# Kernel optimization log

Measured on AMD Instinct MI355X. Metric: run time of the kernel, lower is better.

## Reference

```python
import jax, jax.numpy as jnp
import numpy as np

B, T, D = 4, 2048, 2048
NUM_EXPERTS = 64
TOP_K = 2


def setup_inputs() -> dict:
    key = jax.random.key(0)
    k_x, k_n, k_wg, k_wn = jax.random.split(key, 4)
    x = jax.random.normal(k_x, (B, T, D), dtype=jnp.float32)
    noise_eps = jax.random.normal(k_n, (B, T, NUM_EXPERTS), dtype=jnp.float32)
    # nn.Linear(D, E, bias=False): weight [E, D]; store transposed [D, E] for einsum
    scale = 1.0 / np.sqrt(D)
    w_gate = jax.random.uniform(k_wg, (D, NUM_EXPERTS), jnp.float32, -scale, scale)
    w_noise = jax.random.uniform(k_wn, (D, NUM_EXPERTS), jnp.float32, -scale, scale)
    return {"x": x, "noise_eps": noise_eps, "w_gate": w_gate, "w_noise": w_noise}


def reference(x, noise_eps, w_gate, w_noise):
    # gate + noisy logits: softplus(w_noise(x)) * randn_like (noise_eps passed in)
    logits = jnp.einsum("btd,de->bte", x, w_gate)
    noise = jax.nn.softplus(jnp.einsum("btd,de->bte", x, w_noise)) * noise_eps
    logits = logits + noise

    # top-k over experts
    top_k_logits, top_k_indices = jax.lax.top_k(logits, TOP_K)  # [B,T,K]

    # scatter(-inf fill) + softmax == softmax over top-k values scattered into E slots
    one_hot = jax.nn.one_hot(top_k_indices, NUM_EXPERTS, dtype=logits.dtype)  # [B,T,K,E]
    router_probs = jnp.einsum("btk,btke->bte", jax.nn.softmax(top_k_logits, axis=-1), one_hot)

    # per-expert mask: [num_tokens, K, E] -> permute(1,0,2) -> [K, num_tokens, E]
    exp_mask = one_hot.reshape(B * T, TOP_K, NUM_EXPERTS).transpose(1, 0, 2).astype(jnp.int32)
    return router_probs, top_k_indices, exp_mask
```

## Files before the change

kernel.cpp:

```cpp
#include <hip/hip_runtime.h>
#include <math.h>

#define DD     2048
#define EE     64
#define NTOK   8192
#define BM     32
#define KSPLIT 4
#define NKS    16

#define PROB_OFF 0
#define IDX_OFF  524288
#define MASK_OFF 540672
#define MASK_K_STRIDE (NTOK * EE)

typedef __bf16 bf16x8 __attribute__((ext_vector_type(8)));
typedef float  f32x16 __attribute__((ext_vector_type(16)));

__device__ __forceinline__ unsigned f2bf_rne(float f) {
  unsigned u = __float_as_uint(f);
  return (u + 0x7fffu + ((u >> 16) & 1u)) >> 16;
}
__device__ __forceinline__ float bf2f(unsigned h) {
  return __uint_as_float(h << 16);
}

__global__ __launch_bounds__(256) void prep_w(
    const float* __restrict__ wg, const float* __restrict__ wn,
    unsigned char* __restrict__ wsb)
{
  const int t  = blockIdx.x * 256 + threadIdx.x;
  const int l  = t & 63;
  const int nt = (t >> 6) & 3;
  const int g  = t >> 8;
  const int colg = nt * 32 + (l & 31);
  const int kb   = g * 16 + 8 * (l >> 5);
  const float* wsrc = (colg < EE) ? (wg + colg) : (wn + (colg - EE));

  unsigned hv[8], lv[8];
#pragma unroll
  for (int i = 0; i < 8; ++i) {
    const float v = wsrc[(size_t)(kb + i) * EE];
    const unsigned h = f2bf_rne(v);
    hv[i] = h;
    lv[i] = f2bf_rne(v - bf2f(h));
  }
  uint4 hq, lq;
  hq.x = hv[0] | (hv[1] << 16); hq.y = hv[2] | (hv[3] << 16);
  hq.z = hv[4] | (hv[5] << 16); hq.w = hv[6] | (hv[7] << 16);
  lq.x = lv[0] | (lv[1] << 16); lq.y = lv[2] | (lv[3] << 16);
  lq.z = lv[4] | (lv[5] << 16); lq.w = lv[6] | (lv[7] << 16);

  const size_t base = ((size_t)(g * 4 + nt) * 2) * 1024 + (size_t)l * 16;
  *reinterpret_cast<uint4*>(wsb + base)        = hq;
  *reinterpret_cast<uint4*>(wsb + base + 1024) = lq;
}

union BF8 { bf16x8 v; ushort u[8]; };

__device__ __forceinline__ void cvt_hilo(const float4& a, const float4& b,
                                         bf16x8& hi, bf16x8& lo) {
  const float f[8] = {a.x, a.y, a.z, a.w, b.x, b.y, b.z, b.w};
  BF8 H, L;
#pragma unroll
  for (int i = 0; i < 8; ++i) {
    const unsigned u = __float_as_uint(f[i]);
    H.u[i] = (ushort)(u >> 16);
    L.v[i] = (__bf16)(f[i] - __uint_as_float(u & 0xffff0000u));
  }
  hi = H.v; lo = L.v;
}

__device__ __forceinline__ bf16x8 bc(const uint4& q) {
  return __builtin_bit_cast(bf16x8, q);
}

__global__ __launch_bounds__(256, 4) void router_gemm(
    const float* __restrict__ x,
    const unsigned char* __restrict__ wsb,
    float* __restrict__ part)
{
  __shared__ float Lp[BM][128];

  const int tid  = threadIdx.x;
  const int w    = tid >> 6;
  const int lane = tid & 63;
  const int nt2  = w & 1;
  const int kq   = w >> 1;
  const int tok0 = blockIdx.x * BM;
  const int ks   = blockIdx.y;

  const int kbase = ks * 512 + kq * 256;
  const float* xp = x + (size_t)(tok0 + (lane & 31)) * DD
                      + kbase + 8 * (lane >> 5);
  const unsigned char* bp = wsb
      + ((size_t)((kbase >> 4) * 4 + 2 * nt2)) * 2048 + (size_t)lane * 16;

  f32x16 a0 = {0.f,0.f,0.f,0.f,0.f,0.f,0.f,0.f,0.f,0.f,0.f,0.f,0.f,0.f,0.f,0.f};
  f32x16 a1 = a0;

#pragma unroll
  for (int s = 0; s < NKS; ++s) {
    const float* p = xp + 16 * s;
    const float4 xa = *reinterpret_cast<const float4*>(p);
    const float4 xb = *reinterpret_cast<const float4*>(p + 4);
    const unsigned char* q = bp + (size_t)8192 * s;
    const uint4 bh0 = *reinterpret_cast<const uint4*>(q);
    const uint4 bl0 = *reinterpret_cast<const uint4*>(q + 1024);
    const uint4 bh1 = *reinterpret_cast<const uint4*>(q + 2048);
    const uint4 bl1 = *reinterpret_cast<const uint4*>(q + 3072);

    bf16x8 ahi, alo;
    cvt_hilo(xa, xb, ahi, alo);
    a0 = __builtin_amdgcn_mfma_f32_32x32x16_bf16(ahi, bc(bh0), a0, 0, 0, 0);
    a0 = __builtin_amdgcn_mfma_f32_32x32x16_bf16(ahi, bc(bl0), a0, 0, 0, 0);
    a0 = __builtin_amdgcn_mfma_f32_32x32x16_bf16(alo, bc(bh0), a0, 0, 0, 0);
    a1 = __builtin_amdgcn_mfma_f32_32x32x16_bf16(ahi, bc(bh1), a1, 0, 0, 0);
    a1 = __builtin_amdgcn_mfma_f32_32x32x16_bf16(ahi, bc(bl1), a1, 0, 0, 0);
    a1 = __builtin_amdgcn_mfma_f32_32x32x16_bf16(alo, bc(bh1), a1, 0, 0, 0);
  }

  const int ccol  = 64 * nt2 + (lane & 31);
  const int crow0 = 4 * (lane >> 5);
  if (kq == 0) {
#pragma unroll
    for (int q = 0; q < 16; ++q) {
      const int row = (q & 3) + 8 * (q >> 2) + crow0;
      Lp[row][ccol]      = a0[q];
      Lp[row][ccol + 32] = a1[q];
    }
  }
  __syncthreads();
  if (kq == 1) {
#pragma unroll
    for (int q = 0; q < 16; ++q) {
      const int row = (q & 3) + 8 * (q >> 2) + crow0;
      Lp[row][ccol]      += a0[q];
      Lp[row][ccol + 32] += a1[q];
    }
  }
  __syncthreads();

#pragma unroll
  for (int rr = 0; rr < 8; ++rr) {
    const int r = 8 * w + rr;
    const float2 v = *reinterpret_cast<const float2*>(&Lp[r][2 * lane]);
    *reinterpret_cast<float2*>(
        part + ((size_t)(tok0 + r) * KSPLIT + ks) * 128 + 2 * lane) = v;
  }
}

__global__ __launch_bounds__(256) void router_epilogue(
    const float* __restrict__ part,
    const float* __restrict__ noise_eps,
    float* __restrict__ out)
{
  const int t    = blockIdx.x * 4 + (threadIdx.x >> 6);
  const int lane = threadIdx.x & 63;

  const float* p = part + (size_t)t * KSPLIT * 128;
  float g = 0.0f, nraw = 0.0f;
#pragma unroll
  for (int s = 0; s < KSPLIT; ++s) {
    g    += p[s * 128 + lane];
    nraw += p[s * 128 + EE + lane];
  }
  const float ep = noise_eps[(size_t)t * EE + lane];

  const float sp = fmaxf(nraw, 0.0f) + log1pf(expf(-fabsf(nraw)));
  const float z  = fmaf(sp, ep, g);

  float v1 = z; int i1 = lane;
#pragma unroll
  for (int off = 32; off >= 1; off >>= 1) {
    const float ov = __shfl_xor(v1, off, 64);
    const int   oi = __shfl_xor(i1, off, 64);
    if (ov > v1 || (ov == v1 && oi < i1)) { v1 = ov; i1 = oi; }
  }
  float v2 = (lane == i1) ? -INFINITY : z; int i2 = lane;
#pragma unroll
  for (int off = 32; off >= 1; off >>= 1) {
    const float ov = __shfl_xor(v2, off, 64);
    const int   oi = __shfl_xor(i2, off, 64);
    if (ov > v2 || (ov == v2 && oi < i2)) { v2 = ov; i2 = oi; }
  }

  const float e2 = expf(v2 - v1);
  const float denom = 1.0f + e2;
  const float p1 = 1.0f / denom;
  const float p2 = e2 / denom;

  out[PROB_OFF + (size_t)t * EE + lane] =
      (lane == i1) ? p1 : ((lane == i2) ? p2 : 0.0f);

  if (lane == 0) {
    out[IDX_OFF + t * 2 + 0] = (float)i1;
    out[IDX_OFF + t * 2 + 1] = (float)i2;
  }

  out[MASK_OFF + 0 * MASK_K_STRIDE + (size_t)t * EE + lane] = (lane == i1) ? 1.0f : 0.0f;
  out[MASK_OFF + 1 * MASK_K_STRIDE + (size_t)t * EE + lane] = (lane == i2) ? 1.0f : 0.0f;
}

extern "C" void kernel_launch(void* const* d_in, const int* in_sizes, int n_in,
                              void* d_out, int out_size, void* d_ws, size_t ws_size,
                              hipStream_t stream) {
  const float* x   = (const float*)d_in[0];
  const float* eps = (const float*)d_in[1];
  const float* wg  = (const float*)d_in[2];
  const float* wn  = (const float*)d_in[3];

  unsigned char* wsb = (unsigned char*)d_ws;
  float* part = (float*)(wsb + (1 << 20));

  prep_w<<<dim3(128), dim3(256), 0, stream>>>(wg, wn, wsb);
  router_gemm<<<dim3(NTOK / BM, KSPLIT), dim3(256), 0, stream>>>(x, wsb, part);
  router_epilogue<<<dim3(NTOK / 4), dim3(256), 0, stream>>>(part, eps,
                                                            (float*)d_out);
}
```

Before: 137.1 us.

## Fuse router GEMM and top-k epilogue into one 1024-thread kernel

Merges the split-K GEMM and the top-k/softmax epilogue into a single kernel. Each 32-token block now uses 16 waves, each covering a 128-wide K slice and all 128 output columns. Partial sums are reduced through a 4-slab shared-memory buffer over four synchronised phases, after which each wave computes the epilogue for two tokens. This removes the global partial-sum buffer round trip and one kernel launch. In exchange it uses large 1024-thread blocks with more accumulator registers, which may lower occupancy, and adds four block barriers.

```diff
diff --git a/kernel.cpp b/kernel.cpp
--- a/kernel.cpp
+++ b/kernel.cpp
@@ -1,12 +1,12 @@
 #include <hip/hip_runtime.h>
 #include <math.h>
 
-#define DD     2048
-#define EE     64
-#define NTOK   8192
-#define BM     32
-#define KSPLIT 4
-#define NKS    16
+#define DD    2048
+#define EE    64
+#define NTOK  8192
+#define BM    32
+#define NKH   16
+#define NKS   8
 
 #define PROB_OFF 0
 #define IDX_OFF  524288
@@ -74,29 +74,26 @@
   return __builtin_bit_cast(bf16x8, q);
 }
 
-__global__ __launch_bounds__(256, 4) void router_gemm(
+__global__ __launch_bounds__(1024) void router_fused(
     const float* __restrict__ x,
+    const float* __restrict__ noise_eps,
     const unsigned char* __restrict__ wsb,
-    float* __restrict__ part)
+    float* __restrict__ out)
 {
-  __shared__ float Lp[BM][128];
+  __shared__ float Lp[4][BM][128];
 
   const int tid  = threadIdx.x;
-  const int w    = tid >> 6;
+  const int wid  = tid >> 6;
   const int lane = tid & 63;
-  const int nt2  = w & 1;
-  const int kq   = w >> 1;
+  const int kh   = wid;
   const int tok0 = blockIdx.x * BM;
-  const int ks   = blockIdx.y;
-
-  const int kbase = ks * 512 + kq * 256;
+
   const float* xp = x + (size_t)(tok0 + (lane & 31)) * DD
-                      + kbase + 8 * (lane >> 5);
-  const unsigned char* bp = wsb
-      + ((size_t)((kbase >> 4) * 4 + 2 * nt2)) * 2048 + (size_t)lane * 16;
+                      + kh * 128 + 8 * (lane >> 5);
+  const unsigned char* bp = wsb + (size_t)kh * 65536 + (size_t)lane * 16;
 
   f32x16 a0 = {0.f,0.f,0.f,0.f,0.f,0.f,0.f,0.f,0.f,0.f,0.f,0.f,0.f,0.f,0.f,0.f};
-  f32x16 a1 = a0;
+  f32x16 a1 = a0, a2 = a0, a3 = a0;
 
 #pragma unroll
   for (int s = 0; s < NKS; ++s) {
@@ -104,101 +101,111 @@
     const float4 xa = *reinterpret_cast<const float4*>(p);
     const float4 xb = *reinterpret_cast<const float4*>(p + 4);
     const unsigned char* q = bp + (size_t)8192 * s;
-    const uint4 bh0 = *reinterpret_cast<const uint4*>(q);
-    const uint4 bl0 = *reinterpret_cast<const uint4*>(q + 1024);
-    const uint4 bh1 = *reinterpret_cast<const uint4*>(q + 2048);
-    const uint4 bl1 = *reinterpret_cast<const uint4*>(q + 3072);
 
     bf16x8 ahi, alo;
     cvt_hilo(xa, xb, ahi, alo);
-    a0 = __builtin_amdgcn_mfma_f32_32x32x16_bf16(ahi, bc(bh0), a0, 0, 0, 0);
-    a0 = __builtin_amdgcn_mfma_f32_32x32x16_bf16(ahi, bc(bl0), a0, 0, 0, 0);
-    a0 = __builtin_amdgcn_mfma_f32_32x32x16_bf16(alo, bc(bh0), a0, 0, 0, 0);
-    a1 = __builtin_amdgcn_mfma_f32_32x32x16_bf16(ahi, bc(bh1), a1, 0, 0, 0);
-    a1 = __builtin_amdgcn_mfma_f32_32x32x16_bf16(ahi, bc(bl1), a1, 0, 0, 0);
-    a1 = __builtin_amdgcn_mfma_f32_32x32x16_bf16(alo, bc(bh1), a1, 0, 0, 0);
-  }
-
-  const int ccol  = 64 * nt2 + (lane & 31);
+
+    {
+      const uint4 bh0 = *reinterpret_cast<const uint4*>(q);
+      const uint4 bl0 = *reinterpret_cast<const uint4*>(q + 1024);
+      const uint4 bh1 = *reinterpret_cast<const uint4*>(q + 2048);
+      const uint4 bl1 = *reinterpret_cast<const uint4*>(q + 3072);
+      a0 = __builtin_amdgcn_mfma_f32_32x32x16_bf16(ahi, bc(bh0), a0, 0, 0, 0);
+      a0 = __builtin_amdgcn_mfma_f32_32x32x16_bf16(ahi, bc(bl0), a0, 0, 0, 0);
+      a0 = __builtin_amdgcn_mfma_f32_32x32x16_bf16(alo, bc(bh0), a0, 0, 0, 0);
+      a1 = __builtin_amdgcn_mfma_f32_32x32x16_bf16(ahi, bc(bh1), a1, 0, 0, 0);
+      a1 = __builtin_amdgcn_mfma_f32_32x32x16_bf16(ahi, bc(bl1), a1, 0, 0, 0);
+      a1 = __builtin_amdgcn_mfma_f32_32x32x16_bf16(alo, bc(bh1), a1, 0, 0, 0);
+    }
+    {
+      const uint4 bh2 = *reinterpret_cast<const uint4*>(q + 4096);
+      const uint4 bl2 = *reinterpret_cast<const uint4*>(q + 5120);
+      const uint4 bh3 = *reinterpret_cast<const uint4*>(q + 6144);
+      const uint4 bl3 = *reinterpret_cast<const uint4*>(q + 7168);
+      a2 = __builtin_amdgcn_mfma_f32_32x32x16_bf16(ahi, bc(bh2), a2, 0, 0, 0);
+      a2 = __builtin_amdgcn_mfma_f32_32x32x16_bf16(ahi, bc(bl2), a2, 0, 0, 0);
+      a2 = __builtin_amdgcn_mfma_f32_32x32x16_bf16(alo, bc(bh2), a2, 0, 0, 0);
+      a3 = __builtin_amdgcn_mfma_f32_32x32x16_bf16(ahi, bc(bh3), a3, 0, 0, 0);
+      a3 = __builtin_amdgcn_mfma_f32_32x32x16_bf16(ahi, bc(bl3), a3, 0, 0, 0);
+      a3 = __builtin_amdgcn_mfma_f32_32x32x16_bf16(alo, bc(bh3), a3, 0, 0, 0);
+    }
+  }
+
+  const int slab  = kh & 3;
+  const int phase = kh >> 2;
+  const int ccol  = lane & 31;
   const int crow0 = 4 * (lane >> 5);
-  if (kq == 0) {
-#pragma unroll
-    for (int q = 0; q < 16; ++q) {
-      const int row = (q & 3) + 8 * (q >> 2) + crow0;
-      Lp[row][ccol]      = a0[q];
-      Lp[row][ccol + 32] = a1[q];
-    }
-  }
-  __syncthreads();
-  if (kq == 1) {
-#pragma unroll
-    for (int q = 0; q < 16; ++q) {
-      const int row = (q & 3) + 8 * (q >> 2) + crow0;
-      Lp[row][ccol]      += a0[q];
-      Lp[row][ccol + 32] += a1[q];
-    }
-  }
-  __syncthreads();
-
-#pragma unroll
-  for (int rr = 0; rr < 8; ++rr) {
-    const int r = 8 * w + rr;
-    const float2 v = *reinterpret_cast<const float2*>(&Lp[r][2 * lane]);
-    *reinterpret_cast<float2*>(
-        part + ((size_t)(tok0 + r) * KSPLIT + ks) * 128 + 2 * lane) = v;
-  }
-}
-
-__global__ __launch_bounds__(256) void router_epilogue(
-    const float* __restrict__ part,
-    const float* __restrict__ noise_eps,
-    float* __restrict__ out)
-{
-  const int t    = blockIdx.x * 4 + (threadIdx.x >> 6);
-  const int lane = threadIdx.x & 63;
-
-  const float* p = part + (size_t)t * KSPLIT * 128;
-  float g = 0.0f, nraw = 0.0f;
-#pragma unroll
-  for (int s = 0; s < KSPLIT; ++s) {
-    g    += p[s * 128 + lane];
-    nraw += p[s * 128 + EE + lane];
-  }
-  const float ep = noise_eps[(size_t)t * EE + lane];
-
-  const float sp = fmaxf(nraw, 0.0f) + log1pf(expf(-fabsf(nraw)));
-  const float z  = fmaf(sp, ep, g);
-
-  float v1 = z; int i1 = lane;
-#pragma unroll
-  for (int off = 32; off >= 1; off >>= 1) {
-    const float ov = __shfl_xor(v1, off, 64);
-    const int   oi = __shfl_xor(i1, off, 64);
-    if (ov > v1 || (ov == v1 && oi < i1)) { v1 = ov; i1 = oi; }
-  }
-  float v2 = (lane == i1) ? -INFINITY : z; int i2 = lane;
-#pragma unroll
-  for (int off = 32; off >= 1; off >>= 1) {
-    const float ov = __shfl_xor(v2, off, 64);
-    const int   oi = __shfl_xor(i2, off, 64);
-    if (ov > v2 || (ov == v2 && oi < i2)) { v2 = ov; i2 = oi; }
-  }
-
-  const float e2 = expf(v2 - v1);
-  const float denom = 1.0f + e2;
-  const float p1 = 1.0f / denom;
-  const float p2 = e2 / denom;
-
-  out[PROB_OFF + (size_t)t * EE + lane] =
-      (lane == i1) ? p1 : ((lane == i2) ? p2 : 0.0f);
-
-  if (lane == 0) {
-    out[IDX_OFF + t * 2 + 0] = (float)i1;
-    out[IDX_OFF + t * 2 + 1] = (float)i2;
-  }
-
-  out[MASK_OFF + 0 * MASK_K_STRIDE + (size_t)t * EE + lane] = (lane == i1) ? 1.0f : 0.0f;
-  out[MASK_OFF + 1 * MASK_K_STRIDE + (size_t)t * EE + lane] = (lane == i2) ? 1.0f : 0.0f;
+#pragma unroll
+  for (int ph = 0; ph < 4; ++ph) {
+    if (phase == ph) {
+      if (ph == 0) {
+#pragma unroll
+        for (int q = 0; q < 16; ++q) {
+          const int row = (q & 3) + 8 * (q >> 2) + crow0;
+          Lp[slab][row][ccol]      = a0[q];
+          Lp[slab][row][ccol + 32] = a1[q];
+          Lp[slab][row][ccol + 64] = a2[q];
+          Lp[slab][row][ccol + 96] = a3[q];
+        }
+      } else {
+#pragma unroll
+        for (int q = 0; q < 16; ++q) {
+          const int row = (q & 3) + 8 * (q >> 2) + crow0;
+          Lp[slab][row][ccol]      += a0[q];
+          Lp[slab][row][ccol + 32] += a1[q];
+          Lp[slab][row][ccol + 64] += a2[q];
+          Lp[slab][row][ccol + 96] += a3[q];
+        }
+      }
+    }
+    __syncthreads();
+  }
+
+#pragma unroll
+  for (int it = 0; it < 2; ++it) {
+    const int tl  = wid * 2 + it;
+    const int tok = tok0 + tl;
+
+    const float g    = Lp[0][tl][lane] + Lp[1][tl][lane]
+                     + Lp[2][tl][lane] + Lp[3][tl][lane];
+    const float nraw = Lp[0][tl][64 + lane] + Lp[1][tl][64 + lane]
+                     + Lp[2][tl][64 + lane] + Lp[3][tl][64 + lane];
+    const float ep   = noise_eps[(size_t)tok * EE + lane];
+
+    const float sp = fmaxf(nraw, 0.0f) + log1pf(expf(-fabsf(nraw)));
+    const float z  = fmaf(sp, ep, g);
+
+    float v1 = z; int i1 = lane;
+#pragma unroll
+    for (int off = 32; off >= 1; off >>= 1) {
+      const float ov = __shfl_xor(v1, off, 64);
+      const int   oi = __shfl_xor(i1, off, 64);
+      if (ov > v1 || (ov == v1 && oi < i1)) { v1 = ov; i1 = oi; }
+    }
+    float v2 = (lane == i1) ? -INFINITY : z; int i2 = lane;
+#pragma unroll
+    for (int off = 32; off >= 1; off >>= 1) {
+      const float ov = __shfl_xor(v2, off, 64);
+      const int   oi = __shfl_xor(i2, off, 64);
+      if (ov > v2 || (ov == v2 && oi < i2)) { v2 = ov; i2 = oi; }
+    }
+
+    const float e2 = expf(v2 - v1);
+    const float denom = 1.0f + e2;
+    const float p1 = 1.0f / denom;
+    const float p2 = e2 / denom;
+
+    out[PROB_OFF + (size_t)tok * EE + lane] =
+        (lane == i1) ? p1 : ((lane == i2) ? p2 : 0.0f);
+    if (lane == 0) {
+      out[IDX_OFF + tok * 2 + 0] = (float)i1;
+      out[IDX_OFF + tok * 2 + 1] = (float)i2;
+    }
+    out[MASK_OFF + 0 * MASK_K_STRIDE + (size_t)tok * EE + lane] =
+        (lane == i1) ? 1.0f : 0.0f;
+    out[MASK_OFF + 1 * MASK_K_STRIDE + (size_t)tok * EE + lane] =
+        (lane == i2) ? 1.0f : 0.0f;
+  }
 }
 
 extern "C" void kernel_launch(void* const* d_in, const int* in_sizes, int n_in,
@@ -208,12 +215,9 @@
   const float* eps = (const float*)d_in[1];
   const float* wg  = (const float*)d_in[2];
   const float* wn  = (const float*)d_in[3];
-
   unsigned char* wsb = (unsigned char*)d_ws;
-  float* part = (float*)(wsb + (1 << 20));
 
   prep_w<<<dim3(128), dim3(256), 0, stream>>>(wg, wn, wsb);
-  router_gemm<<<dim3(NTOK / BM, KSPLIT), dim3(256), 0, stream>>>(x, wsb, part);
-  router_epilogue<<<dim3(NTOK / 4), dim3(256), 0, stream>>>(part, eps,
-                                                            (float*)d_out);
-}
+  router_fused<<<dim3(NTOK / BM), dim3(1024), 0, stream>>>(x, eps, wsb,
+                                                           (float*)d_out);
+}
```

Result: faster. 126.5 us (-7.7%).

## Stage GEMM tiles through double-buffered LDS with direct global-to-LDS loads

Applied to the files above, without the earlier changes.

The router GEMM now uses global_load_lds to copy x and the packed weight tiles into double-buffered shared memory, prefetching the next 64-wide K chunk while MFMAs run on the current one. The x tile is XOR-swizzled to avoid bank conflicts. The K split drops from 4 to 2 and each wave now owns one 32-column tile instead of splitting K across waves, which removes the in-block reduction. The cost is 80KB of LDS per block, which limits occupancy to about two blocks per CU, plus a sync per chunk.

```diff
diff --git a/kernel.cpp b/kernel.cpp
--- a/kernel.cpp
+++ b/kernel.cpp
@@ -5,14 +5,20 @@
 #define EE     64
 #define NTOK   8192
 #define BM     32
-#define KSPLIT 4
-#define NKS    16
+#define KSPLIT 2
+#define KHALF  1024
+#define BK     64
+#define NCH    (KHALF / BK)
 
 #define PROB_OFF 0
 #define IDX_OFF  524288
 #define MASK_OFF 540672
 #define MASK_K_STRIDE (NTOK * EE)
 
+#define XBUF_OFF(b) ((b) * 8192)
+#define BBUF_OFF(b) (16384 + (b) * 32768)
+#define LDS_BYTES   81920
+
 typedef __bf16 bf16x8 __attribute__((ext_vector_type(8)));
 typedef float  f32x16 __attribute__((ext_vector_type(16)));
 
@@ -22,6 +28,13 @@
 }
 __device__ __forceinline__ float bf2f(unsigned h) {
   return __uint_as_float(h << 16);
+}
+
+__device__ __forceinline__ void gl_lds16(const void* g, void* l) {
+  __builtin_amdgcn_global_load_lds(
+      (const __attribute__((address_space(1))) unsigned int*)g,
+      (__attribute__((address_space(3))) unsigned int*)l,
+      16, 0, 0);
 }
 
 __global__ __launch_bounds__(256) void prep_w(
@@ -74,76 +87,92 @@
   return __builtin_bit_cast(bf16x8, q);
 }
 
-__global__ __launch_bounds__(256, 4) void router_gemm(
+__global__ __launch_bounds__(256, 2) void router_gemm(
     const float* __restrict__ x,
     const unsigned char* __restrict__ wsb,
     float* __restrict__ part)
 {
-  __shared__ float Lp[BM][128];
+  __shared__ unsigned char lds[LDS_BYTES];
 
   const int tid  = threadIdx.x;
-  const int w    = tid >> 6;
+  const int wid  = tid >> 6;
   const int lane = tid & 63;
-  const int nt2  = w & 1;
-  const int kq   = w >> 1;
+  const int nt   = wid;
   const int tok0 = blockIdx.x * BM;
   const int ks   = blockIdx.y;
 
-  const int kbase = ks * 512 + kq * 256;
-  const float* xp = x + (size_t)(tok0 + (lane & 31)) * DD
-                      + kbase + 8 * (lane >> 5);
-  const unsigned char* bp = wsb
-      + ((size_t)((kbase >> 4) * 4 + 2 * nt2)) * 2048 + (size_t)lane * 16;
-
-  f32x16 a0 = {0.f,0.f,0.f,0.f,0.f,0.f,0.f,0.f,0.f,0.f,0.f,0.f,0.f,0.f,0.f,0.f};
-  f32x16 a1 = a0;
-
-#pragma unroll
-  for (int s = 0; s < NKS; ++s) {
-    const float* p = xp + 16 * s;
-    const float4 xa = *reinterpret_cast<const float4*>(p);
-    const float4 xb = *reinterpret_cast<const float4*>(p + 4);
-    const unsigned char* q = bp + (size_t)8192 * s;
-    const uint4 bh0 = *reinterpret_cast<const uint4*>(q);
-    const uint4 bl0 = *reinterpret_cast<const uint4*>(q + 1024);
-    const uint4 bh1 = *reinterpret_cast<const uint4*>(q + 2048);
-    const uint4 bl1 = *reinterpret_cast<const uint4*>(q + 3072);
-
-    bf16x8 ahi, alo;
-    cvt_hilo(xa, xb, ahi, alo);
-    a0 = __builtin_amdgcn_mfma_f32_32x32x16_bf16(ahi, bc(bh0), a0, 0, 0, 0);
-    a0 = __builtin_amdgcn_mfma_f32_32x32x16_bf16(ahi, bc(bl0), a0, 0, 0, 0);
-    a0 = __builtin_amdgcn_mfma_f32_32x32x16_bf16(alo, bc(bh0), a0, 0, 0, 0);
-    a1 = __builtin_amdgcn_mfma_f32_32x32x16_bf16(ahi, bc(bh1), a1, 0, 0, 0);
-    a1 = __builtin_amdgcn_mfma_f32_32x32x16_bf16(ahi, bc(bl1), a1, 0, 0, 0);
-    a1 = __builtin_amdgcn_mfma_f32_32x32x16_bf16(alo, bc(bh1), a1, 0, 0, 0);
-  }
-
-  const int ccol  = 64 * nt2 + (lane & 31);
-  const int crow0 = 4 * (lane >> 5);
-  if (kq == 0) {
-#pragma unroll
-    for (int q = 0; q < 16; ++q) {
-      const int row = (q & 3) + 8 * (q >> 2) + crow0;
-      Lp[row][ccol]      = a0[q];
-      Lp[row][ccol + 32] = a1[q];
+  const int row0 = tid >> 4;
+  const int sl0  = tid & 15;
+  const float* xsrc0 = x + (size_t)(tok0 + row0) * DD + ks * KHALF
+                         + ((sl0 ^ (row0 & 15)) << 2);
+  const float* xsrc1 = x + (size_t)(tok0 + row0 + 16) * DD + ks * KHALF
+                         + ((sl0 ^ ((row0 + 16) & 15)) << 2);
+  const unsigned char* bsrc = wsb + (size_t)ks * (KHALF / 16) * 8192
+                                  + (size_t)tid * 16;
+
+  const int arow = lane & 31;
+  const int atl  = lane >> 5;
+  const int aswz = (arow & 15) << 4;
+
+  f32x16 acc = {0.f,0.f,0.f,0.f,0.f,0.f,0.f,0.f,
+                0.f,0.f,0.f,0.f,0.f,0.f,0.f,0.f};
+
+  {
+    gl_lds16(xsrc0, &lds[XBUF_OFF(0) + tid * 16]);
+    gl_lds16(xsrc1, &lds[XBUF_OFF(0) + 4096 + tid * 16]);
+#pragma unroll
+    for (int j = 0; j < 8; ++j)
+      gl_lds16(bsrc + j * 4096, &lds[BBUF_OFF(0) + j * 4096 + tid * 16]);
+  }
+  __syncthreads();
+
+  for (int c = 0; c < NCH; ++c) {
+    const int cb = c & 1;
+
+    if (c + 1 < NCH) {
+      const int nb = cb ^ 1;
+      gl_lds16(xsrc0 + (c + 1) * BK, &lds[XBUF_OFF(nb) + tid * 16]);
+      gl_lds16(xsrc1 + (c + 1) * BK, &lds[XBUF_OFF(nb) + 4096 + tid * 16]);
+      const unsigned char* bs = bsrc + (size_t)(c + 1) * 32768;
+#pragma unroll
+      for (int j = 0; j < 8; ++j)
+        gl_lds16(bs + j * 4096, &lds[BBUF_OFF(nb) + j * 4096 + tid * 16]);
     }
+
+    const unsigned char* xb = &lds[XBUF_OFF(cb)];
+    const unsigned char* bb = &lds[BBUF_OFF(cb)];
+#pragma unroll
+    for (int s = 0; s < 4; ++s) {
+      const int koff = s * 64 + atl * 32;
+      const float4 xa = *reinterpret_cast<const float4*>(
+          xb + arow * 256 + (koff ^ aswz));
+      const float4 xv = *reinterpret_cast<const float4*>(
+          xb + arow * 256 + ((koff + 16) ^ aswz));
+      const unsigned char* q = bb + (s * 4 + nt) * 2048 + lane * 16;
+      const uint4 bh = *reinterpret_cast<const uint4*>(q);
+      const uint4 bl = *reinterpret_cast<const uint4*>(q + 1024);
+
+      bf16x8 ahi, alo;
+      cvt_hilo(xa, xv, ahi, alo);
+      acc = __builtin_amdgcn_mfma_f32_32x32x16_bf16(ahi, bc(bh), acc, 0, 0, 0);
+      acc = __builtin_amdgcn_mfma_f32_32x32x16_bf16(ahi, bc(bl), acc, 0, 0, 0);
+      acc = __builtin_amdgcn_mfma_f32_32x32x16_bf16(alo, bc(bh), acc, 0, 0, 0);
+    }
+    __syncthreads();
+  }
+
+  float* Lp = reinterpret_cast<float*>(lds);
+  const int ccol = nt * 32 + (lane & 31);
+#pragma unroll
+  for (int q = 0; q < 16; ++q) {
+    const int r = (q & 3) + 8 * (q >> 2) + 4 * atl;
+    Lp[r * 128 + ccol] = acc[q];
   }
   __syncthreads();
-  if (kq == 1) {
-#pragma unroll
-    for (int q = 0; q < 16; ++q) {
-      const int row = (q & 3) + 8 * (q >> 2) + crow0;
-      Lp[row][ccol]      += a0[q];
-      Lp[row][ccol + 32] += a1[q];
-    }
-  }
-  __syncthreads();
-
 #pragma unroll
   for (int rr = 0; rr < 8; ++rr) {
-    const int r = 8 * w + rr;
-    const float2 v = *reinterpret_cast<const float2*>(&Lp[r][2 * lane]);
+    const int r = 8 * wid + rr;
+    const float2 v = *reinterpret_cast<const float2*>(&Lp[r * 128 + 2 * lane]);
     *reinterpret_cast<float2*>(
         part + ((size_t)(tok0 + r) * KSPLIT + ks) * 128 + 2 * lane) = v;
   }
```

New measurement: 125.9 us. -8.1%, faster.
